# Performance work log

Measured on AMD Instinct MI355X. Metric: run time of the kernel, lower is better.

The kernel has to match this reference:

```python
import jax, jax.numpy as jnp
import numpy as np

NEG_INF = -1e9  # fp32-safe mask value for non-edges
ALPHA = 0.2     # LeakyReLU negative slope


def setup_inputs() -> dict:
    key = jax.random.key(0)
    k1, k2, k3, k4, k5 = jax.random.split(key, 5)
    N, F_in, H, F_out = 4096, 512, 8, 64
    features = jax.random.normal(k1, (N, F_in), dtype=jnp.float32)
    adjacency_matrix = jax.random.randint(k2, (N, N), 0, 2, dtype=jnp.int32)
    W = jax.random.normal(k3, (H, F_in, F_out), dtype=jnp.float32) * (F_in ** -0.5)
    a_src = jax.random.normal(k4, (H, F_out), dtype=jnp.float32) * (F_out ** -0.5)
    a_dst = jax.random.normal(k5, (H, F_out), dtype=jnp.float32) * (F_out ** -0.5)
    return {"features": features, "adjacency_matrix": adjacency_matrix,
            "W": W, "a_src": a_src, "a_dst": a_dst}


def reference(features, adjacency_matrix, W, a_src, a_dst):
    # Per-head linear projection: [H, N, F_out]
    Wh = jnp.einsum('nf,hfo->hno', features, W)
    # Attention logits e_ij = LeakyReLU(a_src . Wh_i + a_dst . Wh_j)
    src = jnp.einsum('hno,ho->hn', Wh, a_src)  # [H, N]
    dst = jnp.einsum('hno,ho->hn', Wh, a_dst)  # [H, N]
    e = jax.nn.leaky_relu(src[:, :, None] + dst[:, None, :], ALPHA)  # [H, N, N]
    mask = (adjacency_matrix > 0)[None, :, :]
    e = jnp.where(mask, e, jnp.asarray(NEG_INF, e.dtype))
    attn = jax.nn.softmax(e, axis=-1)  # adjacency-masked row softmax
    h = jnp.einsum('hij,hjo->hio', attn, Wh)  # [H, N, F_out]
    h = jax.nn.elu(h)
    # concat=True: torch.cat over feature dim -> [N, H*F_out]
    return jnp.transpose(h, (1, 0, 2)).reshape(h.shape[1], -1)
```

## Files before the change

### kernel.cpp

```cpp
#include <hip/hip_runtime.h>
#include <hip/hip_bf16.h>

typedef __bf16 bf16x8 __attribute__((ext_vector_type(8)));
typedef _Float16 f16x8 __attribute__((ext_vector_type(8)));
typedef _Float16 f16x2 __attribute__((ext_vector_type(2)));
typedef float  f32x4  __attribute__((ext_vector_type(4)));
typedef unsigned short u16x8 __attribute__((ext_vector_type(8)));
typedef unsigned short us4   __attribute__((ext_vector_type(4)));

#define HH    8
#define NN    4096
#define FIN   512
#define FOUT  64
#define ALPHA 0.2f

__global__ __launch_bounds__(256) void k_transpose_w(
    const float* __restrict__ Wsrc, __hip_bfloat16* __restrict__ WT) {
    __shared__ __hip_bfloat16 lt[64][65];
    const int h  = blockIdx.x >> 3;
    const int f0 = (blockIdx.x & 7) * 64;
    const int tid = threadIdx.x;
#pragma unroll
    for (int p = 0; p < 16; ++p) {
        int f = p * 4 + (tid >> 6);
        int o = tid & 63;
        lt[f][o] = __float2bfloat16(Wsrc[((size_t)h * FIN + f0 + f) * FOUT + o]);
    }
    __syncthreads();
#pragma unroll
    for (int p = 0; p < 16; ++p) {
        int o = p * 4 + (tid >> 6);
        int f = tid & 63;
        WT[((size_t)h * FOUT + o) * FIN + f0 + f] = lt[f][o];
    }
}

__global__ __launch_bounds__(256) void k_prep(
    const int* __restrict__ adj,
    unsigned* __restrict__ maskdst, int mstride,
    const float* __restrict__ feat,
    const __hip_bfloat16* __restrict__ WT,
    const float* __restrict__ a_src,
    const float* __restrict__ a_dst,
    unsigned short* __restrict__ WhT,
    float* __restrict__ srcv,
    unsigned short* __restrict__ Ebf, unsigned short* __restrict__ Fbf) {
    __shared__ alignas(16) __hip_bfloat16 lfeat[32][520];

    const int tid = threadIdx.x;

    if (blockIdx.x < 2048) {
        const size_t base = (size_t)blockIdx.x * 8192;
        unsigned m = 0;
#pragma unroll
        for (int p = 0; p < 8; ++p) {
            int4 v = *(const int4*)(adj + base + tid * 32 + p * 4);
            m |= (unsigned)(v.x > 0) << (p * 4);
            m |= (unsigned)(v.y > 0) << (p * 4 + 1);
            m |= (unsigned)(v.z > 0) << (p * 4 + 2);
            m |= (unsigned)(v.w > 0) << (p * 4 + 3);
        }
        __syncthreads();
        maskdst[(size_t)blockIdx.x * mstride + tid] = m;
        return;
    }

    const int pb   = blockIdx.x - 2048;
    const int tile = pb & 127;
    const int hgy  = pb >> 7;

#pragma unroll
    for (int p = 0; p < 16; ++p) {
        int idx  = p * 256 + tid;
        int row  = idx >> 7;
        int col4 = (idx & 127) * 4;
        float4 f = *(const float4*)(feat + (size_t)(tile * 32 + row) * FIN + col4);
        __hip_bfloat16* dst = &lfeat[row][col4];
        dst[0] = __float2bfloat16(f.x); dst[1] = __float2bfloat16(f.y);
        dst[2] = __float2bfloat16(f.z); dst[3] = __float2bfloat16(f.w);
    }
    __syncthreads();

    const int h     = hgy * 4 + (tid >> 6);
    const int lane  = tid & 63;
    const int row16 = lane & 15;
    const int quad  = lane >> 4;

    const unsigned short* WTu = (const unsigned short*)WT + (size_t)h * FOUT * FIN;

    f32x4 acc[2][4] = {};
    for (int k0 = 0; k0 < FIN; k0 += 32) {
        bf16x8 a0 = *(const bf16x8*)&lfeat[row16][k0 + quad * 8];
        bf16x8 a1 = *(const bf16x8*)&lfeat[16 + row16][k0 + quad * 8];
#pragma unroll
        for (int ot = 0; ot < 4; ++ot) {
            bf16x8 b = *(const bf16x8*)(WTu + (size_t)(ot * 16 + row16) * FIN + k0 + quad * 8);
            acc[0][ot] = __builtin_amdgcn_mfma_f32_16x16x32_bf16(a0, b, acc[0][ot], 0, 0, 0);
            acc[1][ot] = __builtin_amdgcn_mfma_f32_16x16x32_bf16(a1, b, acc[1][ot], 0, 0, 0);
        }
    }

#pragma unroll
    for (int g = 0; g < 2; ++g)
#pragma unroll
        for (int ot = 0; ot < 4; ++ot) {
            us4 u;
#pragma unroll
            for (int r = 0; r < 4; ++r)
                u[r] = __builtin_bit_cast(unsigned short, (_Float16)acc[g][ot][r]);
            *(us4*)(WhT + (((size_t)(h * 128 + tile) * 64 + ot * 16 + row16) << 5)
                        + g * 16 + quad * 4) = u;
        }

    float asv[4], adv[4];
#pragma unroll
    for (int ot = 0; ot < 4; ++ot) {
        asv[ot] = a_src[h * FOUT + ot * 16 + row16];
        adv[ot] = a_dst[h * FOUT + ot * 16 + row16];
    }
#pragma unroll
    for (int g = 0; g < 2; ++g)
#pragma unroll
        for (int r = 0; r < 4; ++r) {
            float ss = 0.f, dd = 0.f;
#pragma unroll
            for (int ot = 0; ot < 4; ++ot) {
                ss += acc[g][ot][r] * asv[ot];
                dd += acc[g][ot][r] * adv[ot];
            }
            ss += __shfl_xor(ss, 1); ss += __shfl_xor(ss, 2);
            ss += __shfl_xor(ss, 4); ss += __shfl_xor(ss, 8);
            dd += __shfl_xor(dd, 1); dd += __shfl_xor(dd, 2);
            dd += __shfl_xor(dd, 4); dd += __shfl_xor(dd, 8);
            if (row16 == 0) {
                int n = tile * 32 + g * 16 + quad * 4 + r;
                srcv[h * NN + n] = ss;
                _Float16 e = (_Float16)__expf(dd);
                _Float16 f = (_Float16)__expf(ALPHA * dd);
                Ebf[h * NN + n] = __builtin_bit_cast(unsigned short, e);
                Fbf[h * NN + n] = __builtin_bit_cast(unsigned short, f);
            }
        }
}

__global__ __launch_bounds__(256, 3) void k_flash(
    const unsigned* __restrict__ maskp, int mstride,
    const float* __restrict__ srcv,
    const unsigned short* __restrict__ Ebf,
    const unsigned short* __restrict__ Fbf,
    const unsigned short* __restrict__ WhT,
    float* __restrict__ out) {
    __shared__ float st[2][64 * 68];
    __shared__ float lds_l[2][64];

    unsigned* lmask = (unsigned*)&st[0][0];

    const int tid   = threadIdx.x;
    const int seg   = tid >> 6;
    const int lane  = tid & 63;
    const int row16 = lane & 15;
    const int quad  = lane >> 4;
    const int shl   = quad * 8;
    const int tile  = blockIdx.x;
    const int h     = blockIdx.y;

#pragma unroll
    for (int p = 0; p < 8; ++p) {
        int tt = tid + p * 256;
        int c  = tt >> 6;
        int o  = (tt & 63) * 16;
        int4 v = *(const int4*)((const char*)maskp
                                + ((size_t)(tile * 32 + c) * mstride) * 4 + o);
        int row = c * 2 + (o >> 9);
        int dw  = (o & 511) >> 2;
        *(int4*)&lmask[row * 132 + dw] = v;
    }
    __syncthreads();

    f16x2 Es2[4], Fs2[4];
#pragma unroll
    for (int g = 0; g < 4; ++g) {
        float si = srcv[h * NN + tile * 64 + g * 16 + row16];
        _Float16 e = (_Float16)__expf(si);
        _Float16 f = (_Float16)__expf(ALPHA * si);
        Es2[g][0] = e; Es2[g][1] = e;
        Fs2[g][0] = f; Fs2[g][1] = f;
    }
    const int mbase = row16 * 132 + seg * 32;

    const unsigned short* Eb  = Ebf + h * NN + seg * 1024;
    const unsigned short* Fb  = Fbf + h * NN + seg * 1024;
    const unsigned short* whh = WhT + (size_t)h * FOUT * NN;

    f32x4 acc[4][4] = {};
    float lsum[4]   = {};
    const f16x2 ones2 = {(_Float16)1.0f, (_Float16)1.0f};

    auto LOAD = [&](f16x8& ev_, f16x8& fv_, f16x8* b_, unsigned* m_, int tt) {
        const int jj = tt * 32 + shl;
        const size_t jb = (size_t)(seg * 32 + tt) << 11;
        ev_ = *(const f16x8*)(Eb + jj);
        fv_ = *(const f16x8*)(Fb + jj);
#pragma unroll
        for (int ot = 0; ot < 4; ++ot)
            b_[ot] = *(const f16x8*)(whh + jb + (ot * 16 + row16) * 32 + quad * 8);
#pragma unroll
        for (int g = 0; g < 4; ++g)
            m_[g] = lmask[mbase + g * 2112 + tt];
    };

    auto COMP = [&](const f16x8& ev_, const f16x8& fv_,
                    const f16x8* b_, const unsigned* m_) {
        union { f16x8 v8; f16x2 h2[4]; } evu, fvu;
        evu.v8 = ev_; fvu.v8 = fv_;
#pragma unroll
        for (int g = 0; g < 4; ++g) {
            unsigned mb = m_[g] >> shl;
            union { f16x8 v8; unsigned w[4]; } au;
#pragma unroll
            for (int kk = 0; kk < 4; ++kk) {
                f16x2 t0 = evu.h2[kk] * Es2[g];
                f16x2 t1 = fvu.h2[kk] * Fs2[g];
                f16x2 p2 = __builtin_elementwise_max(t0, t1);
                unsigned lo = (unsigned)__builtin_amdgcn_sbfe((int)mb, 2 * kk, 1);
                unsigned hi = (unsigned)__builtin_amdgcn_sbfe((int)mb, 2 * kk + 1, 1);
                unsigned w  = (lo & 0xFFFFu) | (hi & 0xFFFF0000u);
                unsigned pw = __builtin_bit_cast(unsigned, p2) & w;
                f16x2 mp2   = __builtin_bit_cast(f16x2, pw);
                au.w[kk] = pw;
#if __has_builtin(__builtin_amdgcn_fdot2)
                lsum[g] = __builtin_amdgcn_fdot2(mp2, ones2, lsum[g], false);
#else
                lsum[g] += (float)mp2[0] + (float)mp2[1];
#endif
            }
            __builtin_amdgcn_s_setprio(1);
#pragma unroll
            for (int ot = 0; ot < 4; ++ot)
                acc[g][ot] = __builtin_amdgcn_mfma_f32_16x16x32_f16(au.v8, b_[ot], acc[g][ot], 0, 0, 0);
            __builtin_amdgcn_s_setprio(0);
        }
    };

    int t0 = ((seg * 8) + ((tile & 1) << 2)) & 31;
    f16x8 evA, fvA, bA[4]; unsigned mA[4];
    f16x8 evB, fvB, bB[4]; unsigned mB[4];
    LOAD(evA, fvA, bA, mA, t0);

#pragma unroll 1
    for (int i = 0; i < 16; ++i) {
        const int t1 = (t0 + 1) & 31;
        LOAD(evB, fvB, bB, mB, t1);
        COMP(evA, fvA, bA, mA);
        const int t2 = (t0 + 2) & 31;
        LOAD(evA, fvA, bA, mA, t2);
        COMP(evB, fvB, bB, mB);
        t0 = t2;
    }

#pragma unroll
    for (int g = 0; g < 4; ++g) {
        lsum[g] += __shfl_xor(lsum[g], 16);
        lsum[g] += __shfl_xor(lsum[g], 32);
    }

    __syncthreads();

    auto stash = [&](int buf) {
#pragma unroll
        for (int g = 0; g < 4; ++g)
#pragma unroll
            for (int ot = 0; ot < 4; ++ot)
#pragma unroll
                for (int r = 0; r < 4; ++r)
                    st[buf][(g * 16 + quad * 4 + r) * 68 + ot * 16 + row16] = acc[g][ot][r];
        if (quad == 0)
#pragma unroll
            for (int g = 0; g < 4; ++g)
                lds_l[buf][g * 16 + row16] = lsum[g];
    };
    auto addin = [&](int buf) {
#pragma unroll
        for (int g = 0; g < 4; ++g) {
#pragma unroll
            for (int ot = 0; ot < 4; ++ot)
#pragma unroll
                for (int r = 0; r < 4; ++r)
                    acc[g][ot][r] += st[buf][(g * 16 + quad * 4 + r) * 68 + ot * 16 + row16];
            lsum[g] += lds_l[buf][g * 16 + row16];
        }
    };

    if (seg == 1) stash(0);
    if (seg == 3) stash(1);
    __syncthreads();
    if (seg == 0) addin(0);
    if (seg == 2) addin(1);
    __syncthreads();
    if (seg == 2) stash(0);
    __syncthreads();
    if (seg == 0) {
        addin(0);
#pragma unroll
        for (int g = 0; g < 4; ++g)
#pragma unroll
            for (int r = 0; r < 4; ++r) {
                int   qr  = quad * 4 + r;
                float l   = __shfl(lsum[g], qr);
                float rl  = 1.0f / l;
#pragma unroll
                for (int ot = 0; ot < 4; ++ot) {
                    float v = acc[g][ot][r] * rl;
                    float y = v > 0.f ? v : __expf(v) - 1.f;
                    st[0][(g * 16 + qr) * 68 + ot * 16 + row16] = y;
                }
            }
    }
    __syncthreads();
#pragma unroll
    for (int p = 0; p < 4; ++p) {
        int f    = tid + p * 256;
        int row  = f >> 4;
        int col4 = (f & 15) * 4;
        float4 v = *(const float4*)&st[0][row * 68 + col4];
        *(float4*)&out[(size_t)(tile * 64 + row) * (HH * FOUT) + h * FOUT + col4] = v;
    }
}

extern "C" void kernel_launch(void* const* d_in, const int* in_sizes, int n_in,
                              void* d_out, int out_size, void* d_ws, size_t ws_size,
                              hipStream_t stream) {
    const float* features = (const float*)d_in[0];
    int*         adj      = (int*)d_in[1];
    const float* W        = (const float*)d_in[2];
    const float* a_src    = (const float*)d_in[3];
    const float* a_dst    = (const float*)d_in[4];
    float*       out      = (float*)d_out;

    char* ws = (char*)d_ws;
    __hip_bfloat16* WT   = (__hip_bfloat16*)(ws);
    unsigned short* WhT  = (unsigned short*)(ws + (512 << 10));
    float*          srcv = (float*)(ws + (512 << 10) + (4 << 20));
    unsigned short* Ebf  = (unsigned short*)(ws + (512 << 10) + (4 << 20) + (128 << 10));
    unsigned short* Fbf  = (unsigned short*)(ws + (512 << 10) + (4 << 20) + (192 << 10));

    const size_t mask_off = (512 << 10) + (4 << 20) + (256 << 10);
    unsigned* maskp; int mstride;
    if (ws_size >= mask_off + (2u << 20)) {
        maskp   = (unsigned*)(ws + mask_off);
        mstride = 256;
    } else {
        maskp   = (unsigned*)adj;
        mstride = 8192;
    }

    k_transpose_w<<<dim3(64), 256, 0, stream>>>(W, WT);
    k_prep<<<dim3(2048 + 256), 256, 0, stream>>>(adj, maskp, mstride,
                                                 features, WT, a_src, a_dst,
                                                 WhT, srcv, Ebf, Fbf);
    k_flash<<<dim3(64, 8), 256, 0, stream>>>(maskp, mstride, srcv, Ebf, Fbf,
                                             WhT, out);
}
```

Baseline: 153.9 us.

## Coalesce adjacency mask loads, reorder prep blocks, and k-block the W layout

Adjacency packing now has consecutive threads read consecutive int4s, builds 32-bit mask words with wave shuffles and LDS, and then writes them out, instead of each thread striding across 128 bytes. Projection blocks are moved to the front of the grid so the MFMA work is scheduled before the mask-packing blocks. The transposed W is stored in 32-wide k-blocks so each MFMA B-operand load reads a contiguous 4KB chunk. The intent is to improve global memory coalescing, at the cost of extra shuffles and an LDS round trip.

```diff
diff --git a/kernel.cpp b/kernel.cpp
--- a/kernel.cpp
+++ b/kernel.cpp
@@ -31,7 +31,8 @@
     for (int p = 0; p < 16; ++p) {
         int o = p * 4 + (tid >> 6);
         int f = tid & 63;
-        WT[((size_t)h * FOUT + o) * FIN + f0 + f] = lt[f][o];
+        int gf = f0 + f;
+        WT[(((size_t)h * 16 + (gf >> 5)) * 64 + o) * 32 + (gf & 31)] = lt[f][o];
     }
 }
 
@@ -49,23 +50,31 @@
 
     const int tid = threadIdx.x;
 
-    if (blockIdx.x < 2048) {
-        const size_t base = (size_t)blockIdx.x * 8192;
-        unsigned m = 0;
-#pragma unroll
-        for (int p = 0; p < 8; ++p) {
-            int4 v = *(const int4*)(adj + base + tid * 32 + p * 4);
-            m |= (unsigned)(v.x > 0) << (p * 4);
-            m |= (unsigned)(v.y > 0) << (p * 4 + 1);
-            m |= (unsigned)(v.z > 0) << (p * 4 + 2);
-            m |= (unsigned)(v.w > 0) << (p * 4 + 3);
-        }
+    if (blockIdx.x >= 256) {
+        const int b = blockIdx.x - 256;
+        const size_t base = (size_t)b * 8192;
+        unsigned* lbuf = (unsigned*)&lfeat[0][0];
+        const int l = tid & 63;
+        const int w = tid >> 6;
+        unsigned keep = 0;
+#pragma unroll
+        for (int i = 0; i < 8; ++i) {
+            int4 v = *(const int4*)(adj + base + (size_t)(i * 256 + tid) * 4);
+            unsigned nib = (unsigned)(v.x > 0) | ((unsigned)(v.y > 0) << 1)
+                         | ((unsigned)(v.z > 0) << 2) | ((unsigned)(v.w > 0) << 3);
+            unsigned vv = nib << ((l & 7) * 4);
+            vv |= __shfl_xor(vv, 1);
+            vv |= __shfl_xor(vv, 2);
+            vv |= __shfl_xor(vv, 4);
+            keep = ((l & 7) == i) ? vv : keep;
+        }
+        lbuf[(l & 7) * 32 + w * 8 + (l >> 3)] = keep;
         __syncthreads();
-        maskdst[(size_t)blockIdx.x * mstride + tid] = m;
+        maskdst[(size_t)b * mstride + tid] = lbuf[tid];
         return;
     }
 
-    const int pb   = blockIdx.x - 2048;
+    const int pb   = blockIdx.x;
     const int tile = pb & 127;
     const int hgy  = pb >> 7;
 
@@ -86,15 +95,16 @@
     const int row16 = lane & 15;
     const int quad  = lane >> 4;
 
-    const unsigned short* WTu = (const unsigned short*)WT + (size_t)h * FOUT * FIN;
+    const unsigned short* WTu = (const unsigned short*)WT + (size_t)h * 16 * 2048;
 
     f32x4 acc[2][4] = {};
     for (int k0 = 0; k0 < FIN; k0 += 32) {
         bf16x8 a0 = *(const bf16x8*)&lfeat[row16][k0 + quad * 8];
         bf16x8 a1 = *(const bf16x8*)&lfeat[16 + row16][k0 + quad * 8];
+        const unsigned short* wkb = WTu + (size_t)(k0 >> 5) * 2048;
 #pragma unroll
         for (int ot = 0; ot < 4; ++ot) {
-            bf16x8 b = *(const bf16x8*)(WTu + (size_t)(ot * 16 + row16) * FIN + k0 + quad * 8);
+            bf16x8 b = *(const bf16x8*)(wkb + (ot * 16 + row16) * 32 + quad * 8);
             acc[0][ot] = __builtin_amdgcn_mfma_f32_16x16x32_bf16(a0, b, acc[0][ot], 0, 0, 0);
             acc[1][ot] = __builtin_amdgcn_mfma_f32_16x16x32_bf16(a1, b, acc[1][ot], 0, 0, 0);
         }
```

New measurement: 143.3 us. 6.9% less time.
